# Kernel tuning notes

Hardware: AMD Instinct MI355X
Metric: run time of the kernel (lower is better)

The kernel has to match this reference:

```python
import jax, jax.numpy as jnp
import numpy as np

B, S, HID = 4, 1024, 768
H, D = 12, 32              # attention_head_size = (HID/H)//2
AH = H * D                 # all_head_size = 384
SCALING = D ** (-0.5)


def setup_inputs() -> dict:
    key = jax.random.key(0)
    ks = jax.random.split(key, 6)
    hidden_states = jax.random.normal(ks[0], (B, S, HID), dtype=jnp.float32)
    attention_mask = jnp.zeros((B, 1, 1, S), dtype=jnp.float32)
    init = 0.02
    Wq = jax.random.normal(ks[1], (AH, HID), dtype=jnp.float32) * init
    Wk1 = jax.random.normal(ks[2], (AH, HID), dtype=jnp.float32) * init
    Wk2 = jax.random.normal(ks[3], (AH, HID), dtype=jnp.float32) * init
    Wv = jax.random.normal(ks[4], (AH, HID), dtype=jnp.float32) * init
    bq = jnp.zeros((AH,), jnp.float32)
    bk1 = jnp.zeros((AH,), jnp.float32)
    bk2 = jnp.zeros((AH,), jnp.float32)
    bv = jnp.zeros((AH,), jnp.float32)
    pi = jnp.ones((2, H), jnp.float32) / 2.0
    return {"hidden_states": hidden_states, "attention_mask": attention_mask,
            "Wq": Wq, "bq": bq, "Wk1": Wk1, "bk1": bk1, "Wk2": Wk2, "bk2": bk2,
            "Wv": Wv, "bv": bv, "pi": pi}


def _heads(x):
    # [B,S,AH] -> [B,H,S,D]
    return x.reshape(B, S, H, D).transpose(0, 2, 1, 3)


def _sq_dist(x1, x2):
    # gpytorch Distance._sq_dist (postprocess=False): mean-adjust, then
    # ||x1||^2 + ||x2||^2 - 2 x1 x2^T, clamped at 0.
    adj = x1.mean(axis=-2, keepdims=True)
    x1 = x1 - adj
    x2 = x2 - adj
    n1 = (x1 * x1).sum(-1, keepdims=True)            # [B,H,S,1]
    n2 = (x2 * x2).sum(-1, keepdims=True)            # [B,H,S,1]
    cross = jnp.einsum('bhqd,bhkd->bhqk', x1, x2)    # [B,H,S,S]
    return jnp.maximum(n1 + jnp.swapaxes(n2, -1, -2) - 2.0 * cross, 0.0)


def reference(hidden_states, attention_mask, Wq, bq, Wk1, bk1, Wk2, bk2, Wv, bv, pi):
    q = _heads(hidden_states @ Wq.T + bq)
    k1 = _heads(hidden_states @ Wk1.T + bk1)
    k2 = _heads(hidden_states @ Wk2.T + bk2)
    v = _heads(hidden_states @ Wv.T + bv)

    d1 = -SCALING / 2.0 * _sq_dist(q, k1) + attention_mask
    d2 = -1.5 * SCALING / 2.0 * _sq_dist(q, k2) + attention_mask
    d1 = d1 - d1.max(axis=-1, keepdims=True)
    d2 = d2 - d2.max(axis=-1, keepdims=True)

    pi_c = jnp.clip(pi, 1e-6, 2.0)                   # clamp per original
    scores = (jnp.exp(d1) * pi_c[0][None, :, None, None]
              + jnp.exp(d2) * pi_c[1][None, :, None, None])
    probs = scores / (scores.sum(axis=-1, keepdims=True) + 1e-6)
    # dropout is identity in eval mode
    ctx = jnp.einsum('bhqk,bhkd->bhqd', probs, v)
    ctx = ctx.transpose(0, 2, 1, 3).reshape(B, S, AH)
    return (ctx, probs)
```

## Files before the change

### kernel.cpp

```cpp
#include <hip/hip_runtime.h>
#include <math.h>

#define BB 4
#define SS 1024
#define HH 12
#define DD 32
#define HIDDEN 768
#define AHS 384
#define RQ 8
#define HEAD_ELEMS (SS*DD)
#define CTX_ELEMS (BB*SS*AHS)

__device__ __forceinline__ float clampf(float x, float lo, float hi){ return fminf(fmaxf(x, lo), hi); }

__global__ __launch_bounds__(256)
void proj_kernel(const float* __restrict__ X,
                 const float* __restrict__ W0, const float* __restrict__ b0,
                 const float* __restrict__ W1, const float* __restrict__ b1,
                 const float* __restrict__ W2, const float* __restrict__ b2,
                 const float* __restrict__ W3, const float* __restrict__ b3,
                 float* __restrict__ qo, float* __restrict__ k1o,
                 float* __restrict__ k2o, float* __restrict__ vo)
{
    const int BM = 128, BN = 64, BK = 16;
    __shared__ float Xs[BK][BM + 4];
    __shared__ float Wsh[BK][BN + 4];
    int t  = threadIdx.x;
    int m0 = blockIdx.x * BM;
    int n0 = blockIdx.y * BN;
    int mat = n0 / AHS;
    int c0  = n0 % AHS;
    const float* W    = (mat==0) ? W0 : (mat==1) ? W1 : (mat==2) ? W2 : W3;
    const float* bias = (mat==0) ? b0 : (mat==1) ? b1 : (mat==2) ? b2 : b3;

    int tx = t & 15, ty = t >> 4;
    int lr = t >> 2;
    int lc = (t & 3) << 2;

    float acc[8][4];
    #pragma unroll
    for (int i = 0; i < 8; i++)
        #pragma unroll
        for (int j = 0; j < 4; j++) acc[i][j] = 0.f;

    float4 xa = *(const float4*)(X + (m0 + lr) * HIDDEN + lc);
    float4 xb = *(const float4*)(X + (m0 + 64 + lr) * HIDDEN + lc);
    float4 wa = *(const float4*)(W + (c0 + lr) * HIDDEN + lc);

    for (int k0 = 0; k0 < HIDDEN; k0 += BK) {
        __syncthreads();
        Xs[lc+0][lr] = xa.x; Xs[lc+1][lr] = xa.y; Xs[lc+2][lr] = xa.z; Xs[lc+3][lr] = xa.w;
        Xs[lc+0][64+lr] = xb.x; Xs[lc+1][64+lr] = xb.y; Xs[lc+2][64+lr] = xb.z; Xs[lc+3][64+lr] = xb.w;
        Wsh[lc+0][lr] = wa.x; Wsh[lc+1][lr] = wa.y; Wsh[lc+2][lr] = wa.z; Wsh[lc+3][lr] = wa.w;
        __syncthreads();
        if (k0 + BK < HIDDEN) {
            xa = *(const float4*)(X + (m0 + lr) * HIDDEN + k0 + BK + lc);
            xb = *(const float4*)(X + (m0 + 64 + lr) * HIDDEN + k0 + BK + lc);
            wa = *(const float4*)(W + (c0 + lr) * HIDDEN + k0 + BK + lc);
        }
        #pragma unroll
        for (int kk = 0; kk < BK; kk++) {
            float a[8], w4[4];
            *(float4*)&a[0] = *(const float4*)&Xs[kk][ty << 3];
            *(float4*)&a[4] = *(const float4*)&Xs[kk][(ty << 3) + 4];
            *(float4*)w4    = *(const float4*)&Wsh[kk][tx << 2];
            #pragma unroll
            for (int i = 0; i < 8; i++)
                #pragma unroll
                for (int j = 0; j < 4; j++)
                    acc[i][j] = fmaf(a[i], w4[j], acc[i][j]);
        }
    }

    #pragma unroll
    for (int i = 0; i < 8; i++) {
        int row = m0 + (ty << 3) + i;
        int b_  = row >> 10;
        int s   = row & 1023;
        #pragma unroll
        for (int j = 0; j < 4; j++) {
            int c = c0 + (tx << 2) + j;
            int h = c >> 5, d = c & 31;
            int bh = b_ * HH + h;
            float val = acc[i][j] + bias[c];
            if (mat == 0)      qo [(bh * SS + s) * DD + d] = val;
            else if (mat == 1) k1o[(bh * DD + d) * SS + s] = val;
            else if (mat == 2) k2o[(bh * DD + d) * SS + s] = val;
            else               vo [(bh * SS + s) * DD + d] = val;
        }
    }
}

__global__ __launch_bounds__(256)
void norms_kernel(const float* __restrict__ k1T, const float* __restrict__ k2T,
                  float* __restrict__ n1, float* __restrict__ n2)
{
    int bh = blockIdx.y;
    int s  = blockIdx.x * 256 + threadIdx.x;
    const float* p1 = k1T + bh * HEAD_ELEMS + s;
    const float* p2 = k2T + bh * HEAD_ELEMS + s;
    float a1 = 0.f, a2 = 0.f;
    #pragma unroll
    for (int d = 0; d < DD; d++) {
        float x1 = p1[d * SS]; a1 = fmaf(x1, x1, a1);
        float x2 = p2[d * SS]; a2 = fmaf(x2, x2, a2);
    }
    n1[bh * SS + s] = a1;
    n2[bh * SS + s] = a2;
}

__global__ __launch_bounds__(256, 4)
void attn_fused(const float* __restrict__ qg,  const float* __restrict__ k1T,
                const float* __restrict__ k2T,
                const float* __restrict__ n1g, const float* __restrict__ n2g,
                const float* __restrict__ maskg, const float* __restrict__ pig,
                const float* __restrict__ vg,
                float* __restrict__ probs, float* __restrict__ ctx)
{
    const float A1C = 0.08838834764831845f;
    const float A2C = 0.13258252147247767f;
    __shared__ float p_s[RQ * SS];
    __shared__ float q_s[RQ * DD];
    __shared__ float red1[4][RQ], red2[4][RQ];
    __shared__ float qn_s[RQ];

    int t    = threadIdx.x;
    int lane = t & 63, wid = t >> 6;
    int bh   = blockIdx.y;
    int b    = bh / HH, h = bh - b * HH;
    int s0   = blockIdx.x * RQ;

    q_s[t] = qg[(bh * SS + s0) * DD + t];
    __syncthreads();
    if (t < RQ) {
        float a = 0.f;
        for (int d = 0; d < DD; d++) { float x = q_s[t * DD + d]; a = fmaf(x, x, a); }
        qn_s[t] = a;
    }
    __syncthreads();

    float pi0 = clampf(pig[h],      1e-6f, 2.0f);
    float pi1 = clampf(pig[HH + h], 1e-6f, 2.0f);

    float e1r[4][RQ], e2r[4][RQ];
    float pm1[RQ], pm2[RQ];
    #pragma unroll
    for (int r = 0; r < RQ; r++) { pm1[r] = -3.4e38f; pm2[r] = -3.4e38f; }

    const float* k1p = k1T + bh * HEAD_ELEMS;
    const float* k2p = k2T + bh * HEAD_ELEMS;
    const float* n1p = n1g + bh * SS;
    const float* n2p = n2g + bh * SS;
    const float* mp  = maskg + b * SS;

    #pragma unroll
    for (int j = 0; j < 4; j++) {
        int k = j * 256 + t;
        float n1k = n1p[k], n2k = n2p[k], mk = mp[k];
        float c1[RQ], c2[RQ];
        #pragma unroll
        for (int r = 0; r < RQ; r++) { c1[r] = 0.f; c2[r] = 0.f; }
        #pragma unroll
        for (int d4 = 0; d4 < 8; d4++) {
            float kv1[4], kv2[4];
            #pragma unroll
            for (int dd = 0; dd < 4; dd++) {
                kv1[dd] = k1p[(d4 * 4 + dd) * SS + k];
                kv2[dd] = k2p[(d4 * 4 + dd) * SS + k];
            }
            #pragma unroll
            for (int r = 0; r < RQ; r++) {
                float qv[4];
                *(float4*)qv = *(const float4*)&q_s[r * DD + d4 * 4];
                #pragma unroll
                for (int dd = 0; dd < 4; dd++) {
                    c1[r] = fmaf(qv[dd], kv1[dd], c1[r]);
                    c2[r] = fmaf(qv[dd], kv2[dd], c2[r]);
                }
            }
        }
        #pragma unroll
        for (int r = 0; r < RQ; r++) {
            float qn  = qn_s[r];
            float d1v = fmaxf(fmaf(-2.f, c1[r], qn + n1k), 0.f);
            float d2v = fmaxf(fmaf(-2.f, c2[r], qn + n2k), 0.f);
            float ev1 = fmaf(-A1C, d1v, mk);
            float ev2 = fmaf(-A2C, d2v, mk);
            e1r[j][r] = ev1;
            e2r[j][r] = ev2;
            pm1[r] = fmaxf(pm1[r], ev1);
            pm2[r] = fmaxf(pm2[r], ev2);
        }
    }

    #pragma unroll
    for (int off = 32; off >= 1; off >>= 1)
        #pragma unroll
        for (int r = 0; r < RQ; r++) {
            pm1[r] = fmaxf(pm1[r], __shfl_xor(pm1[r], off));
            pm2[r] = fmaxf(pm2[r], __shfl_xor(pm2[r], off));
        }
    if (lane == 0) {
        #pragma unroll
        for (int r = 0; r < RQ; r++) { red1[wid][r] = pm1[r]; red2[wid][r] = pm2[r]; }
    }
    __syncthreads();
    float m1[RQ], m2[RQ];
    #pragma unroll
    for (int r = 0; r < RQ; r++) {
        m1[r] = fmaxf(fmaxf(red1[0][r], red1[1][r]), fmaxf(red1[2][r], red1[3][r]));
        m2[r] = fmaxf(fmaxf(red2[0][r], red2[1][r]), fmaxf(red2[2][r], red2[3][r]));
    }

    float ps[RQ];
    #pragma unroll
    for (int r = 0; r < RQ; r++) ps[r] = 0.f;
    #pragma unroll
    for (int j = 0; j < 4; j++)
        #pragma unroll
        for (int r = 0; r < RQ; r++) {
            float p = pi0 * __expf(e1r[j][r] - m1[r]) + pi1 * __expf(e2r[j][r] - m2[r]);
            e1r[j][r] = p;
            ps[r] += p;
        }

    #pragma unroll
    for (int off = 32; off >= 1; off >>= 1)
        #pragma unroll
        for (int r = 0; r < RQ; r++) ps[r] += __shfl_xor(ps[r], off);
    __syncthreads();
    if (lane == 0) {
        #pragma unroll
        for (int r = 0; r < RQ; r++) red1[wid][r] = ps[r];
    }
    __syncthreads();
    float inv[RQ];
    #pragma unroll
    for (int r = 0; r < RQ; r++) {
        float sum = red1[0][r] + red1[1][r] + red1[2][r] + red1[3][r];
        inv[r] = 1.0f / (sum + 1e-6f);
    }

    float* prow = probs + (size_t)(bh * SS + s0) * SS;
    #pragma unroll
    for (int j = 0; j < 4; j++) {
        int k = (j << 8) + t;
        float pv8[8];
        #pragma unroll
        for (int r = 0; r < RQ; r++) pv8[r] = e1r[j][r] * inv[r];
        #pragma unroll
        for (int r = 0; r < RQ; r++) prow[(size_t)r * SS + k] = pv8[r];
        int base = (k << 3) ^ (((k >> 5) & 3) << 3);
        *(float4*)&p_s[base]     = *(float4*)&pv8[0];
        *(float4*)&p_s[base + 4] = *(float4*)&pv8[4];
    }
    __syncthreads();

    {
        int ks = t >> 3;
        int c4 = t & 7;
        int swzc = (ks & 3) << 3;
        const float* vp = vg + bh * HEAD_ELEMS + (c4 << 2);
        float4 acc4[RQ];
        #pragma unroll
        for (int r = 0; r < RQ; r++) acc4[r] = make_float4(0.f, 0.f, 0.f, 0.f);
        #pragma unroll 4
        for (int kk = 0; kk < 32; kk++) {
            int k = (ks << 5) + kk;
            int base = (k << 3) ^ swzc;
            float pr[8];
            *(float4*)&pr[0] = *(const float4*)&p_s[base];
            *(float4*)&pr[4] = *(const float4*)&p_s[base + 4];
            float4 vv = *(const float4*)&vp[k << 5];
            #pragma unroll
            for (int r = 0; r < RQ; r++) {
                acc4[r].x = fmaf(pr[r], vv.x, acc4[r].x);
                acc4[r].y = fmaf(pr[r], vv.y, acc4[r].y);
                acc4[r].z = fmaf(pr[r], vv.z, acc4[r].z);
                acc4[r].w = fmaf(pr[r], vv.w, acc4[r].w);
            }
        }
        __syncthreads();
        #pragma unroll
        for (int r = 0; r < RQ; r++)
            *(float4*)&p_s[((ks << 8) + (r << 5) + (c4 << 2)) ^ ((ks & 3) << 3)] = acc4[r];
    }
    __syncthreads();

    {
        int rr = t >> 5, dd = t & 31;
        float o = 0.f;
        #pragma unroll
        for (int s2 = 0; s2 < 32; s2++)
            o += p_s[((s2 << 8) + (rr << 5) + dd) ^ ((s2 & 3) << 3)];
        ctx[((size_t)(b * SS + s0 + rr) * HH + h) * DD + dd] = o;
    }
}

extern "C" void kernel_launch(void* const* d_in, const int* in_sizes, int n_in,
                              void* d_out, int out_size, void* d_ws, size_t ws_size,
                              hipStream_t stream)
{
    const float* hs   = (const float*)d_in[0];
    const float* mask = (const float*)d_in[1];
    const float* Wq   = (const float*)d_in[2];
    const float* bq   = (const float*)d_in[3];
    const float* Wk1  = (const float*)d_in[4];
    const float* bk1  = (const float*)d_in[5];
    const float* Wk2  = (const float*)d_in[6];
    const float* bk2  = (const float*)d_in[7];
    const float* Wv   = (const float*)d_in[8];
    const float* bv   = (const float*)d_in[9];
    const float* pi   = (const float*)d_in[10];

    float* ws   = (float*)d_ws;
    float* q_ws = ws;
    float* v_ws = ws + (size_t)CTX_ELEMS * 1;
    float* k1T  = ws + (size_t)CTX_ELEMS * 2;
    float* k2T  = ws + (size_t)CTX_ELEMS * 3;
    float* n1   = ws + (size_t)CTX_ELEMS * 4;
    float* n2   = n1 + BB * HH * SS;

    float* ctx   = (float*)d_out;
    float* probs = ctx + CTX_ELEMS;

    proj_kernel<<<dim3(32, 24), 256, 0, stream>>>(hs, Wq, bq, Wk1, bk1, Wk2, bk2,
                                                  Wv, bv, q_ws, k1T, k2T, v_ws);
    norms_kernel<<<dim3(SS / 256, BB * HH), 256, 0, stream>>>(k1T, k2T, n1, n2);
    attn_fused<<<dim3(SS / RQ, BB * HH), 256, 0, stream>>>(q_ws, k1T, k2T,
                                                           n1, n2, mask, pi,
                                                           v_ws, probs, ctx);
}
```

Before: 537.6 us.

## Interleave K in d4-major float4 layout, swizzle attention block order, nontemporal stores

Changes the K1/K2 workspace layout from fully transposed [bh][d][s] to [bh][d/4][s][4], so the projection writes and the attention and norm kernels read them as float4 vectors instead of scalars. The attention grid becomes 1D with a block-index swizzle that spreads consecutive blocks across heads, likely aiming at better XCD/L2 locality on the multi-die GPU. Probs and ctx writes use nontemporal stores to avoid polluting cache with the large probs output. The swizzle's locality effect is uncertain, and the h computation now takes the head index modulo HH.

Result: faster. 519.9 us (-3.3%).

```diff
diff --git a/kernel.cpp b/kernel.cpp
--- a/kernel.cpp
+++ b/kernel.cpp
@@ -72,46 +72,59 @@
         }
     }
 
+    int cbase = c0 + (tx << 2);
+    int h  = (cbase >> 5) % HH;
+    int d0 = cbase & 31;
+    int d4 = d0 >> 2;
+    float4 bq4 = *(const float4*)(bias + cbase);
+
     #pragma unroll
     for (int i = 0; i < 8; i++) {
         int row = m0 + (ty << 3) + i;
         int b_  = row >> 10;
         int s   = row & 1023;
-        #pragma unroll
-        for (int j = 0; j < 4; j++) {
-            int c = c0 + (tx << 2) + j;
-            int h = c >> 5, d = c & 31;
-            int bh = b_ * HH + h;
-            float val = acc[i][j] + bias[c];
-            if (mat == 0)      qo [(bh * SS + s) * DD + d] = val;
-            else if (mat == 1) k1o[(bh * DD + d) * SS + s] = val;
-            else if (mat == 2) k2o[(bh * DD + d) * SS + s] = val;
-            else               vo [(bh * SS + s) * DD + d] = val;
-        }
+        int bh  = b_ * HH + h;
+        float4 val;
+        val.x = acc[i][0] + bq4.x;
+        val.y = acc[i][1] + bq4.y;
+        val.z = acc[i][2] + bq4.z;
+        val.w = acc[i][3] + bq4.w;
+        if (mat == 0)
+            *(float4*)&qo[((size_t)(bh * SS + s)) * DD + d0] = val;
+        else if (mat == 1)
+            *(float4*)&k1o[((size_t)(bh * 8 + d4) * SS + s) * 4] = val;
+        else if (mat == 2)
+            *(float4*)&k2o[((size_t)(bh * 8 + d4) * SS + s) * 4] = val;
+        else
+            *(float4*)&vo[((size_t)(bh * SS + s)) * DD + d0] = val;
     }
 }
 
 __global__ __launch_bounds__(256)
-void norms_kernel(const float* __restrict__ k1T, const float* __restrict__ k2T,
+void norms_kernel(const float* __restrict__ k1i, const float* __restrict__ k2i,
                   float* __restrict__ n1, float* __restrict__ n2)
 {
     int bh = blockIdx.y;
     int s  = blockIdx.x * 256 + threadIdx.x;
-    const float* p1 = k1T + bh * HEAD_ELEMS + s;
-    const float* p2 = k2T + bh * HEAD_ELEMS + s;
+    const float* p1 = k1i + (size_t)bh * (8 * SS * 4) + s * 4;
+    const float* p2 = k2i + (size_t)bh * (8 * SS * 4) + s * 4;
     float a1 = 0.f, a2 = 0.f;
     #pragma unroll
-    for (int d = 0; d < DD; d++) {
-        float x1 = p1[d * SS]; a1 = fmaf(x1, x1, a1);
-        float x2 = p2[d * SS]; a2 = fmaf(x2, x2, a2);
+    for (int d4 = 0; d4 < 8; d4++) {
+        float4 v1 = *(const float4*)&p1[(size_t)d4 * SS * 4];
+        float4 v2 = *(const float4*)&p2[(size_t)d4 * SS * 4];
+        a1 = fmaf(v1.x, v1.x, a1); a1 = fmaf(v1.y, v1.y, a1);
+        a1 = fmaf(v1.z, v1.z, a1); a1 = fmaf(v1.w, v1.w, a1);
+        a2 = fmaf(v2.x, v2.x, a2); a2 = fmaf(v2.y, v2.y, a2);
+        a2 = fmaf(v2.z, v2.z, a2); a2 = fmaf(v2.w, v2.w, a2);
     }
     n1[bh * SS + s] = a1;
     n2[bh * SS + s] = a2;
 }
 
 __global__ __launch_bounds__(256, 4)
-void attn_fused(const float* __restrict__ qg,  const float* __restrict__ k1T,
-                const float* __restrict__ k2T,
+void attn_fused(const float* __restrict__ qg,  const float* __restrict__ k1i,
+                const float* __restrict__ k2i,
                 const float* __restrict__ n1g, const float* __restrict__ n2g,
                 const float* __restrict__ maskg, const float* __restrict__ pig,
                 const float* __restrict__ vg,
@@ -126,9 +139,12 @@
 
     int t    = threadIdx.x;
     int lane = t & 63, wid = t >> 6;
-    int bh   = blockIdx.y;
-    int b    = bh / HH, h = bh - b * HH;
-    int s0   = blockIdx.x * RQ;
+
+    int bid = blockIdx.x;
+    int swz = (bid & 7) * 768 + (bid >> 3);
+    int bh  = swz >> 7;
+    int s0  = (swz & 127) * RQ;
+    int b   = bh / HH, h = bh - b * HH;
 
     q_s[t] = qg[(bh * SS + s0) * DD + t];
     __syncthreads();
@@ -147,8 +163,8 @@
     #pragma unroll
     for (int r = 0; r < RQ; r++) { pm1[r] = -3.4e38f; pm2[r] = -3.4e38f; }
 
-    const float* k1p = k1T + bh * HEAD_ELEMS;
-    const float* k2p = k2T + bh * HEAD_ELEMS;
+    const float* k1p = k1i + (size_t)bh * (8 * SS * 4);
+    const float* k2p = k2i + (size_t)bh * (8 * SS * 4);
     const float* n1p = n1g + bh * SS;
     const float* n2p = n2g + bh * SS;
     const float* mp  = maskg + b * SS;
@@ -162,12 +178,10 @@
         for (int r = 0; r < RQ; r++) { c1[r] = 0.f; c2[r] = 0.f; }
         #pragma unroll
         for (int d4 = 0; d4 < 8; d4++) {
-            float kv1[4], kv2[4];
-            #pragma unroll
-            for (int dd = 0; dd < 4; dd++) {
-                kv1[dd] = k1p[(d4 * 4 + dd) * SS + k];
-                kv2[dd] = k2p[(d4 * 4 + dd) * SS + k];
-            }
+            float4 kq1 = *(const float4*)&k1p[((size_t)d4 * SS + k) * 4];
+            float4 kq2 = *(const float4*)&k2p[((size_t)d4 * SS + k) * 4];
+            const float* kv1 = (const float*)&kq1;
+            const float* kv2 = (const float*)&kq2;
             #pragma unroll
             for (int r = 0; r < RQ; r++) {
                 float qv[4];
@@ -249,7 +263,8 @@
         #pragma unroll
         for (int r = 0; r < RQ; r++) pv8[r] = e1r[j][r] * inv[r];
         #pragma unroll
-        for (int r = 0; r < RQ; r++) prow[(size_t)r * SS + k] = pv8[r];
+        for (int r = 0; r < RQ; r++)
+            __builtin_nontemporal_store(pv8[r], &prow[(size_t)r * SS + k]);
         int base = (k << 3) ^ (((k >> 5) & 3) << 3);
         *(float4*)&p_s[base]     = *(float4*)&pv8[0];
         *(float4*)&p_s[base + 4] = *(float4*)&pv8[4];
@@ -293,7 +308,7 @@
         #pragma unroll
         for (int s2 = 0; s2 < 32; s2++)
             o += p_s[((s2 << 8) + (rr << 5) + dd) ^ ((s2 & 3) << 3)];
-        ctx[((size_t)(b * SS + s0 + rr) * HH + h) * DD + dd] = o;
+        __builtin_nontemporal_store(o, &ctx[((size_t)(b * SS + s0 + rr) * HH + h) * DD + dd]);
     }
 }
 
@@ -327,7 +342,7 @@
     proj_kernel<<<dim3(32, 24), 256, 0, stream>>>(hs, Wq, bq, Wk1, bk1, Wk2, bk2,
                                                   Wv, bv, q_ws, k1T, k2T, v_ws);
     norms_kernel<<<dim3(SS / 256, BB * HH), 256, 0, stream>>>(k1T, k2T, n1, n2);
-    attn_fused<<<dim3(SS / RQ, BB * HH), 256, 0, stream>>>(q_ws, k1T, k2T,
-                                                           n1, n2, mask, pi,
-                                                           v_ws, probs, ctx);
+    attn_fused<<<dim3(BB * HH * (SS / RQ)), 256, 0, stream>>>(q_ws, k1T, k2T,
+                                                              n1, n2, mask, pi,
+                                                              v_ws, probs, ctx);
 }
```
